# Kernel optimization log

Hardware: AMD Instinct MI355X
Metric: run time of the kernel (lower is better)

Reference implementation:

```python
import math
import jax, jax.numpy as jnp
import numpy as np

NUM_HEAD = 8
EPS = 1e-5

def _ln(v, w, b):
    m = jnp.mean(v, axis=-1, keepdims=True)
    var = jnp.var(v, axis=-1, keepdims=True)  # biased var, as torch LayerNorm
    return (v - m) * jax.lax.rsqrt(var + EPS) * w + b

def setup_inputs() -> dict:
    key = jax.random.key(0)
    ks = jax.random.split(key, 5)
    B, T, D, L, Hd = 16, 2048, 512, 768, 512
    return {
        "x": jax.random.normal(ks[0], (B, T, D), jnp.float32),
        "xf": jax.random.normal(ks[1], (B, T, L), jnp.float32),
        "norm_w": jnp.ones((D,), jnp.float32),
        "norm_b": jnp.zeros((D,), jnp.float32),
        "tnorm_w": jnp.ones((L,), jnp.float32),
        "tnorm_b": jnp.zeros((L,), jnp.float32),
        "Wq": jax.random.normal(ks[2], (Hd, D), jnp.float32) * (1.0 / math.sqrt(D)),
        "Wk": jax.random.normal(ks[3], (Hd, L), jnp.float32) * (1.0 / math.sqrt(L)),
        "Wv": jax.random.normal(ks[4], (Hd, L), jnp.float32) * (1.0 / math.sqrt(L)),
    }

def reference(x, xf, norm_w, norm_b, tnorm_w, tnorm_b, Wq, Wk, Wv):
    B, T, _ = x.shape
    Hd = Wq.shape[0]
    H = NUM_HEAD
    d = Hd // H
    q = _ln(x, norm_w, norm_b) @ Wq.T                 # B,T,Hd
    xf_n = _ln(xf, tnorm_w, tnorm_b)
    k = xf_n @ Wk.T                                   # B,T,Hd (N == T)
    v = xf_n @ Wv.T                                   # B,T,Hd
    qh = q.reshape(B, T, H, d)
    kh = k.reshape(B, T, H, d)
    vh = v.reshape(B, T, H, d)
    # per-position, per-head dot product gate (no softmax)
    w = jnp.einsum('bthd,bthd->bth', qh, kh) / math.sqrt(d)
    # dropout in eval mode = identity
    y2 = (w[..., None] * vh).reshape(B, T, Hd)
    y1 = ((1.0 - w)[..., None] * qh).reshape(B, T, Hd)
    return (y1, y2)
```

## Files before the change

kernel.cpp:

```cpp
#include <hip/hip_runtime.h>

#define NT 512
#define MT 64

typedef __attribute__((ext_vector_type(8))) short short8;
typedef __attribute__((ext_vector_type(4))) float f32x4;
typedef __attribute__((ext_vector_type(4))) unsigned short u16x4;

__device__ __forceinline__ unsigned short f2bf(float f) {
  unsigned int u = __builtin_bit_cast(unsigned int, f);
  u += 0x7fffu + ((u >> 16) & 1u);
  return (unsigned short)(u >> 16);
}
__device__ __forceinline__ float bf2f(unsigned short h) {
  return __builtin_bit_cast(float, ((unsigned int)h) << 16);
}

__global__ void cvt_weights(const float* __restrict__ wq,
                            const float* __restrict__ wk,
                            const float* __restrict__ wv,
                            unsigned short* __restrict__ o) {
  int stride = gridDim.x * blockDim.x;
  int i0 = blockIdx.x * blockDim.x + threadIdx.x;
  for (int t = i0; t < 32768; t += stride) {
    int lane = t & 63, n = (t >> 6) & 3, kk32 = (t >> 8) & 15, head = t >> 12;
    int row = head * 64 + n * 16 + (lane & 15);
    int k   = kk32 * 32 + (lane >> 4) * 8;
    const float* s = wq + (size_t)row * 512 + k;
    unsigned short* d = o + (size_t)t * 8;
    #pragma unroll
    for (int e = 0; e < 8; ++e) d[e] = f2bf(s[e]);
  }
  for (int t = i0; t < 49152; t += stride) {
    int lane = t & 63, n = (t >> 6) & 3, rem = t >> 8;
    int kk32 = rem % 24, head = rem / 24;
    int row = head * 64 + n * 16 + (lane & 15);
    int k   = kk32 * 32 + (lane >> 4) * 8;
    const float* s = wk + (size_t)row * 768 + k;
    unsigned short* d = o + 262144 + (size_t)t * 8;
    #pragma unroll
    for (int e = 0; e < 8; ++e) d[e] = f2bf(s[e]);
  }
  for (int t = i0; t < 49152; t += stride) {
    int lane = t & 63, n = (t >> 6) & 3, rem = t >> 8;
    int kk32 = rem % 24, head = rem / 24;
    int row = head * 64 + n * 16 + (lane & 15);
    int k   = kk32 * 32 + (lane >> 4) * 8;
    const float* s = wv + (size_t)row * 768 + k;
    unsigned short* d = o + 655360 + (size_t)t * 8;
    #pragma unroll
    for (int e = 0; e < 8; ++e) d[e] = f2bf(s[e]);
  }
}

__global__ __launch_bounds__(NT, 2)
void fused_xattn(const float* __restrict__ x, const float* __restrict__ xf,
                 const float* __restrict__ nw, const float* __restrict__ nb,
                 const float* __restrict__ tw, const float* __restrict__ tb,
                 const unsigned short* __restrict__ wbf,
                 float* __restrict__ out) {
  __shared__ __attribute__((aligned(16))) char ldsX[65536];
  __shared__ __attribute__((aligned(16))) char ldsF[98304];
  const int tid   = threadIdx.x;
  const int lane  = tid & 63;
  const int wid   = tid >> 6;
  const int lr    = lane & 15;
  const int lkb   = (lane >> 4) * 8;
  const int lrow4 = (lane >> 4) * 4;

  const long row0 = (long)blockIdx.x * MT;
  float* __restrict__ y1 = out;
  float* __restrict__ y2 = out + 16777216L;

  {
    const f32x4* g4 = (const f32x4*)nw;
    const f32x4* b4 = (const f32x4*)nb;
    f32x4 g0 = g4[lane], g1 = g4[lane + 64];
    f32x4 c0 = b4[lane], c1 = b4[lane + 64];
    #pragma unroll
    for (int cch = 0; cch < 2; ++cch) {
      f32x4 t0[4], t1[4];
      #pragma unroll
      for (int j = 0; j < 4; ++j) {
        const f32x4* rp = (const f32x4*)(x + (row0 + wid + 8 * (cch * 4 + j)) * 512);
        t0[j] = rp[lane]; t1[j] = rp[lane + 64];
      }
      #pragma unroll
      for (int j = 0; j < 4; ++j) {
        f32x4 a = t0[j], b = t1[j];
        float s  = a.x + a.y + a.z + a.w + b.x + b.y + b.z + b.w;
        float s2 = a.x*a.x + a.y*a.y + a.z*a.z + a.w*a.w
                 + b.x*b.x + b.y*b.y + b.z*b.z + b.w*b.w;
        #pragma unroll
        for (int m = 1; m < 64; m <<= 1) { s += __shfl_xor(s, m, 64); s2 += __shfl_xor(s2, m, 64); }
        float mean = s * (1.0f / 512.0f);
        float var  = s2 * (1.0f / 512.0f) - mean * mean;
        float rs   = rsqrtf(var + 1e-5f);
        u16x4 o0 = { f2bf((a.x - mean) * rs * g0.x + c0.x),
                     f2bf((a.y - mean) * rs * g0.y + c0.y),
                     f2bf((a.z - mean) * rs * g0.z + c0.z),
                     f2bf((a.w - mean) * rs * g0.w + c0.w) };
        u16x4 o1 = { f2bf((b.x - mean) * rs * g1.x + c1.x),
                     f2bf((b.y - mean) * rs * g1.y + c1.y),
                     f2bf((b.z - mean) * rs * g1.z + c1.z),
                     f2bf((b.w - mean) * rs * g1.w + c1.w) };
        int r = wid + 8 * (cch * 4 + j);
        int base = r * 1024, sw = (r & 7) << 4;
        *(u16x4*)(ldsX + ((base +       lane * 8) ^ sw)) = o0;
        *(u16x4*)(ldsX + ((base + 512 + lane * 8) ^ sw)) = o1;
      }
    }
  }
  __syncthreads();

  f32x4 f0[2], f1[2], f2[2];
  #pragma unroll
  for (int j = 0; j < 2; ++j) {
    const f32x4* rp = (const f32x4*)(xf + (row0 + wid + 8 * j) * 768);
    f0[j] = rp[lane]; f1[j] = rp[lane + 64]; f2[j] = rp[lane + 128];
  }

  f32x4 qa[4][4] = {};
  {
    const unsigned short* bq = wbf + wid * 32768 + lane * 8;
    short8 bc[4];
    #pragma unroll
    for (int n = 0; n < 4; ++n) bc[n] = *(const short8*)(bq + n * 512);
    for (int kk = 0; kk < 16; ++kk) {
      short8 a[4];
      #pragma unroll
      for (int m = 0; m < 4; ++m) {
        int row = m * 16 + lr;
        a[m] = *(const short8*)(ldsX + ((row * 1024 + (kk * 32 + lkb) * 2) ^ ((row & 7) << 4)));
      }
      short8 bn[4];
      if (kk < 15) {
        #pragma unroll
        for (int n = 0; n < 4; ++n) bn[n] = *(const short8*)(bq + (kk + 1) * 2048 + n * 512);
      }
      #pragma unroll
      for (int n = 0; n < 4; ++n)
        #pragma unroll
        for (int m = 0; m < 4; ++m)
          qa[m][n] = __builtin_amdgcn_mfma_f32_16x16x32_bf16(a[m], bc[n], qa[m][n], 0, 0, 0);
      if (kk < 15) {
        #pragma unroll
        for (int n = 0; n < 4; ++n) bc[n] = bn[n];
      }
    }
  }

  const f32x4* tg4 = (const f32x4*)tw;
  const f32x4* tb4 = (const f32x4*)tb;
  f32x4 tg0 = tg4[lane], tg1 = tg4[lane + 64], tg2 = tg4[lane + 128];
  f32x4 tc0 = tb4[lane], tc1 = tb4[lane + 64], tc2 = tb4[lane + 128];

#define LNF_CHUNK(c2)                                                          \
  {                                                                            \
    _Pragma("unroll")                                                          \
    for (int j = 0; j < 2; ++j) {                                              \
      f32x4 a = f0[j], b = f1[j], c = f2[j];                                   \
      float s  = a.x + a.y + a.z + a.w + b.x + b.y + b.z + b.w                 \
               + c.x + c.y + c.z + c.w;                                        \
      float s2 = a.x*a.x + a.y*a.y + a.z*a.z + a.w*a.w                         \
               + b.x*b.x + b.y*b.y + b.z*b.z + b.w*b.w                         \
               + c.x*c.x + c.y*c.y + c.z*c.z + c.w*c.w;                        \
      _Pragma("unroll")                                                        \
      for (int m = 1; m < 64; m <<= 1) {                                       \
        s += __shfl_xor(s, m, 64); s2 += __shfl_xor(s2, m, 64);                \
      }                                                                        \
      float mean = s * (1.0f / 768.0f);                                        \
      float var  = s2 * (1.0f / 768.0f) - mean * mean;                         \
      float rs   = rsqrtf(var + 1e-5f);                                        \
      u16x4 o0 = { f2bf((a.x - mean) * rs * tg0.x + tc0.x),                    \
                   f2bf((a.y - mean) * rs * tg0.y + tc0.y),                    \
                   f2bf((a.z - mean) * rs * tg0.z + tc0.z),                    \
                   f2bf((a.w - mean) * rs * tg0.w + tc0.w) };                  \
      u16x4 o1 = { f2bf((b.x - mean) * rs * tg1.x + tc1.x),                    \
                   f2bf((b.y - mean) * rs * tg1.y + tc1.y),                    \
                   f2bf((b.z - mean) * rs * tg1.z + tc1.z),                    \
                   f2bf((b.w - mean) * rs * tg1.w + tc1.w) };                  \
      u16x4 o2 = { f2bf((c.x - mean) * rs * tg2.x + tc2.x),                    \
                   f2bf((c.y - mean) * rs * tg2.y + tc2.y),                    \
                   f2bf((c.z - mean) * rs * tg2.z + tc2.z),                    \
                   f2bf((c.w - mean) * rs * tg2.w + tc2.w) };                  \
      int r = wid + 8 * ((c2) * 2 + j);                                        \
      int base = r * 1536, sw = (r & 7) << 4;                                  \
      *(u16x4*)(ldsF + ((base +        lane * 8) ^ sw)) = o0;                  \
      *(u16x4*)(ldsF + ((base + 512  + lane * 8) ^ sw)) = o1;                  \
      *(u16x4*)(ldsF + ((base + 1024 + lane * 8) ^ sw)) = o2;                  \
    }                                                                          \
  }
#define LDF_CHUNK(c2)                                                          \
  {                                                                            \
    _Pragma("unroll")                                                          \
    for (int j = 0; j < 2; ++j) {                                              \
      const f32x4* rp = (const f32x4*)(xf + (row0 + wid + 8 * ((c2) * 2 + j)) * 768); \
      f0[j] = rp[lane]; f1[j] = rp[lane + 64]; f2[j] = rp[lane + 128];         \
    }                                                                          \
  }

  {
    f32x4 n0[2], n1[2], n2[2];
    #pragma unroll
    for (int j = 0; j < 2; ++j) {
      const f32x4* rp = (const f32x4*)(xf + (row0 + wid + 8 * (2 + j)) * 768);
      n0[j] = rp[lane]; n1[j] = rp[lane + 64]; n2[j] = rp[lane + 128];
    }
    LNF_CHUNK(0)
    #pragma unroll
    for (int j = 0; j < 2; ++j) { f0[j] = n0[j]; f1[j] = n1[j]; f2[j] = n2[j]; }
  }
  __syncthreads();

  {
    unsigned long long* q8 = (unsigned long long*)ldsX;
    #pragma unroll
    for (int m = 0; m < 4; ++m)
      #pragma unroll
      for (int n = 0; n < 4; ++n) {
        unsigned long long v =
            (unsigned long long)f2bf(qa[m][n][0])
          | ((unsigned long long)f2bf(qa[m][n][1]) << 16)
          | ((unsigned long long)f2bf(qa[m][n][2]) << 32)
          | ((unsigned long long)f2bf(qa[m][n][3]) << 48);
        q8[wid * 1024 + (m * 4 + n) * 64 + lane] = v;
      }
  }

  {
    f32x4 n0[2], n1[2], n2[2];
    #pragma unroll
    for (int j = 0; j < 2; ++j) {
      const f32x4* rp = (const f32x4*)(xf + (row0 + wid + 8 * (4 + j)) * 768);
      n0[j] = rp[lane]; n1[j] = rp[lane + 64]; n2[j] = rp[lane + 128];
    }
    LNF_CHUNK(1)
    #pragma unroll
    for (int j = 0; j < 2; ++j) { f0[j] = n0[j]; f1[j] = n1[j]; f2[j] = n2[j]; }
    #pragma unroll
    for (int j = 0; j < 2; ++j) {
      const f32x4* rp = (const f32x4*)(xf + (row0 + wid + 8 * (6 + j)) * 768);
      n0[j] = rp[lane]; n1[j] = rp[lane + 64]; n2[j] = rp[lane + 128];
    }
    LNF_CHUNK(2)
    #pragma unroll
    for (int j = 0; j < 2; ++j) { f0[j] = n0[j]; f1[j] = n1[j]; f2[j] = n2[j]; }
    LNF_CHUNK(3)
  }
  __syncthreads();

  f32x4 ka[4][4] = {}, va[4][4] = {};
  {
    const unsigned short* bk = wbf + 262144 + wid * 49152 + lane * 8;
    const unsigned short* bv = wbf + 655360 + wid * 49152 + lane * 8;
    for (int kk = 0; kk < 24; ++kk) {
      short8 kf[4], vf[4];
      #pragma unroll
      for (int n = 0; n < 4; ++n) {
        kf[n] = *(const short8*)(bk + kk * 2048 + n * 512);
        vf[n] = *(const short8*)(bv + kk * 2048 + n * 512);
      }
      short8 a[4];
      #pragma unroll
      for (int m = 0; m < 4; ++m) {
        int row = m * 16 + lr;
        a[m] = *(const short8*)(ldsF + ((row * 1536 + (kk * 32 + lkb) * 2) ^ ((row & 7) << 4)));
      }
      #pragma unroll
      for (int n = 0; n < 4; ++n)
        #pragma unroll
        for (int m = 0; m < 4; ++m) {
          ka[m][n] = __builtin_amdgcn_mfma_f32_16x16x32_bf16(a[m], kf[n], ka[m][n], 0, 0, 0);
          va[m][n] = __builtin_amdgcn_mfma_f32_16x16x32_bf16(a[m], vf[n], va[m][n], 0, 0, 0);
        }
    }
  }

  unsigned long long q64[4][4];
  {
    const unsigned long long* q8 = (const unsigned long long*)ldsX;
    #pragma unroll
    for (int m = 0; m < 4; ++m)
      #pragma unroll
      for (int n = 0; n < 4; ++n)
        q64[m][n] = q8[wid * 1024 + (m * 4 + n) * 64 + lane];
  }
  float wgt[4][4];
  #pragma unroll
  for (int m = 0; m < 4; ++m) {
    #pragma unroll
    for (int r = 0; r < 4; ++r) {
      float p = 0.0f;
      #pragma unroll
      for (int n = 0; n < 4; ++n)
        p += bf2f((unsigned short)(q64[m][n] >> (16 * r))) * ka[m][n][r];
      #pragma unroll
      for (int msk = 1; msk < 16; msk <<= 1) p += __shfl_xor(p, msk, 64);
      wgt[m][r] = p * 0.125f;
    }
  }
  #pragma unroll
  for (int m = 0; m < 4; ++m) {
    #pragma unroll
    for (int r = 0; r < 4; ++r) {
      float f = 1.0f - wgt[m][r];
      long grow = row0 + m * 16 + lrow4 + r;
      #pragma unroll
      for (int n = 0; n < 4; ++n) {
        int ch = wid * 64 + n * 16 + lr;
        y1[grow * 512 + ch] = f * bf2f((unsigned short)(q64[m][n] >> (16 * r)));
      }
    }
  }
  #pragma unroll
  for (int m = 0; m < 4; ++m) {
    #pragma unroll
    for (int r = 0; r < 4; ++r) {
      float f = wgt[m][r];
      long grow = row0 + m * 16 + lrow4 + r;
      #pragma unroll
      for (int n = 0; n < 4; ++n) {
        int ch = wid * 64 + n * 16 + lr;
        y2[grow * 512 + ch] = f * va[m][n][r];
      }
    }
  }
#undef LNF_CHUNK
#undef LDF_CHUNK
}

extern "C" void kernel_launch(void* const* d_in, const int* in_sizes, int n_in,
                              void* d_out, int out_size, void* d_ws, size_t ws_size,
                              hipStream_t stream) {
  const float* x  = (const float*)d_in[0];
  const float* xf = (const float*)d_in[1];
  const float* nw = (const float*)d_in[2];
  const float* nb = (const float*)d_in[3];
  const float* tw = (const float*)d_in[4];
  const float* tb = (const float*)d_in[5];
  const float* wq = (const float*)d_in[6];
  const float* wk = (const float*)d_in[7];
  const float* wv = (const float*)d_in[8];
  unsigned short* wbf = (unsigned short*)d_ws;

  cvt_weights<<<256, 256, 0, stream>>>(wq, wk, wv, wbf);
  fused_xattn<<<512, NT, 0, stream>>>(x, xf, nw, nb, tw, tb, wbf, (float*)d_out);
}
```

Before: 125.5 us.

## Split K/V projections into column halves and keep packed Q in registers

The Q GEMM loop is fully unrolled with double-buffered weight fragments. The Q accumulator is packed to bf16 pairs in registers, so it no longer round-trips through LDS with an extra barrier. The fused K+V GEMM is split into sequential K and V passes, each over two column halves, with the per-row dot product accumulated as it goes. This reduces live accumulator registers so occupancy can rise or spills drop, at the cost of reading the LDS A-tiles four times instead of once and issuing more, smaller weight loads.

```diff
diff --git a/kernel.cpp b/kernel.cpp
--- a/kernel.cpp
+++ b/kernel.cpp
@@ -123,37 +123,76 @@
   f32x4 qa[4][4] = {};
   {
     const unsigned short* bq = wbf + wid * 32768 + lane * 8;
-    short8 bc[4];
-    #pragma unroll
-    for (int n = 0; n < 4; ++n) bc[n] = *(const short8*)(bq + n * 512);
-    for (int kk = 0; kk < 16; ++kk) {
-      short8 a[4];
-      #pragma unroll
-      for (int m = 0; m < 4; ++m) {
-        int row = m * 16 + lr;
-        a[m] = *(const short8*)(ldsX + ((row * 1024 + (kk * 32 + lkb) * 2) ^ ((row & 7) << 4)));
+    short8 b0[4], b1[4];
+    #pragma unroll
+    for (int n = 0; n < 4; ++n) {
+      b0[n] = *(const short8*)(bq + 0 * 2048 + n * 512);
+      b1[n] = *(const short8*)(bq + 1 * 2048 + n * 512);
+    }
+    #pragma unroll
+    for (int p = 0; p < 8; ++p) {
+      {
+        short8 a[4];
+        #pragma unroll
+        for (int m = 0; m < 4; ++m) {
+          int row = m * 16 + lr;
+          a[m] = *(const short8*)(ldsX + ((row * 1024 + ((2 * p) * 32 + lkb) * 2) ^ ((row & 7) << 4)));
+        }
+        short8 nb[4];
+        if (p < 7) {
+          #pragma unroll
+          for (int n = 0; n < 4; ++n) nb[n] = *(const short8*)(bq + (2 * p + 2) * 2048 + n * 512);
+        }
+        #pragma unroll
+        for (int n = 0; n < 4; ++n)
+          #pragma unroll
+          for (int m = 0; m < 4; ++m)
+            qa[m][n] = __builtin_amdgcn_mfma_f32_16x16x32_bf16(a[m], b0[n], qa[m][n], 0, 0, 0);
+        if (p < 7) {
+          #pragma unroll
+          for (int n = 0; n < 4; ++n) b0[n] = nb[n];
+        }
       }
-      short8 bn[4];
-      if (kk < 15) {
+      {
+        short8 a[4];
         #pragma unroll
-        for (int n = 0; n < 4; ++n) bn[n] = *(const short8*)(bq + (kk + 1) * 2048 + n * 512);
+        for (int m = 0; m < 4; ++m) {
+          int row = m * 16 + lr;
+          a[m] = *(const short8*)(ldsX + ((row * 1024 + ((2 * p + 1) * 32 + lkb) * 2) ^ ((row & 7) << 4)));
+        }
+        short8 nb[4];
+        if (p < 7) {
+          #pragma unroll
+          for (int n = 0; n < 4; ++n) nb[n] = *(const short8*)(bq + (2 * p + 3) * 2048 + n * 512);
+        }
+        #pragma unroll
+        for (int n = 0; n < 4; ++n)
+          #pragma unroll
+          for (int m = 0; m < 4; ++m)
+            qa[m][n] = __builtin_amdgcn_mfma_f32_16x16x32_bf16(a[m], b1[n], qa[m][n], 0, 0, 0);
+        if (p < 7) {
+          #pragma unroll
+          for (int n = 0; n < 4; ++n) b1[n] = nb[n];
+        }
       }
-      #pragma unroll
-      for (int n = 0; n < 4; ++n)
-        #pragma unroll
-        for (int m = 0; m < 4; ++m)
-          qa[m][n] = __builtin_amdgcn_mfma_f32_16x16x32_bf16(a[m], bc[n], qa[m][n], 0, 0, 0);
-      if (kk < 15) {
-        #pragma unroll
-        for (int n = 0; n < 4; ++n) bc[n] = bn[n];
-      }
-    }
-  }
-
-  const f32x4* tg4 = (const f32x4*)tw;
-  const f32x4* tb4 = (const f32x4*)tb;
-  f32x4 tg0 = tg4[lane], tg1 = tg4[lane + 64], tg2 = tg4[lane + 128];
-  f32x4 tc0 = tb4[lane], tc1 = tb4[lane + 64], tc2 = tb4[lane + 128];
+    }
+  }
+
+  unsigned q32[4][4][2];
+  #pragma unroll
+  for (int m = 0; m < 4; ++m)
+    #pragma unroll
+    for (int n = 0; n < 4; ++n) {
+      q32[m][n][0] = (unsigned)f2bf(qa[m][n][0]) | ((unsigned)f2bf(qa[m][n][1]) << 16);
+      q32[m][n][1] = (unsigned)f2bf(qa[m][n][2]) | ((unsigned)f2bf(qa[m][n][3]) << 16);
+    }
+#define QF(m, n, r) bf2f((unsigned short)(q32[m][n][(r) >> 1] >> (((r) & 1) * 16)))
+
+  {
+    const f32x4* g4 = (const f32x4*)tw;
+    const f32x4* b4 = (const f32x4*)tb;
+    f32x4 tg0 = g4[lane], tg1 = g4[lane + 64], tg2 = g4[lane + 128];
+    f32x4 tc0 = b4[lane], tc1 = b4[lane + 64], tc2 = b4[lane + 128];
 
 #define LNF_CHUNK(c2)                                                          \
   {                                                                            \
@@ -191,16 +230,7 @@
       *(u16x4*)(ldsF + ((base + 1024 + lane * 8) ^ sw)) = o2;                  \
     }                                                                          \
   }
-#define LDF_CHUNK(c2)                                                          \
-  {                                                                            \
-    _Pragma("unroll")                                                          \
-    for (int j = 0; j < 2; ++j) {                                              \
-      const f32x4* rp = (const f32x4*)(xf + (row0 + wid + 8 * ((c2) * 2 + j)) * 768); \
-      f0[j] = rp[lane]; f1[j] = rp[lane + 64]; f2[j] = rp[lane + 128];         \
-    }                                                                          \
-  }
-
-  {
+
     f32x4 n0[2], n1[2], n2[2];
     #pragma unroll
     for (int j = 0; j < 2; ++j) {
@@ -210,26 +240,6 @@
     LNF_CHUNK(0)
     #pragma unroll
     for (int j = 0; j < 2; ++j) { f0[j] = n0[j]; f1[j] = n1[j]; f2[j] = n2[j]; }
-  }
-  __syncthreads();
-
-  {
-    unsigned long long* q8 = (unsigned long long*)ldsX;
-    #pragma unroll
-    for (int m = 0; m < 4; ++m)
-      #pragma unroll
-      for (int n = 0; n < 4; ++n) {
-        unsigned long long v =
-            (unsigned long long)f2bf(qa[m][n][0])
-          | ((unsigned long long)f2bf(qa[m][n][1]) << 16)
-          | ((unsigned long long)f2bf(qa[m][n][2]) << 32)
-          | ((unsigned long long)f2bf(qa[m][n][3]) << 48);
-        q8[wid * 1024 + (m * 4 + n) * 64 + lane] = v;
-      }
-  }
-
-  {
-    f32x4 n0[2], n1[2], n2[2];
     #pragma unroll
     for (int j = 0; j < 2; ++j) {
       const f32x4* rp = (const f32x4*)(xf + (row0 + wid + 8 * (4 + j)) * 768);
@@ -247,59 +257,91 @@
     #pragma unroll
     for (int j = 0; j < 2; ++j) { f0[j] = n0[j]; f1[j] = n1[j]; f2[j] = n2[j]; }
     LNF_CHUNK(3)
+#undef LNF_CHUNK
   }
   __syncthreads();
 
-  f32x4 ka[4][4] = {}, va[4][4] = {};
-  {
-    const unsigned short* bk = wbf + 262144 + wid * 49152 + lane * 8;
-    const unsigned short* bv = wbf + 655360 + wid * 49152 + lane * 8;
-    for (int kk = 0; kk < 24; ++kk) {
-      short8 kf[4], vf[4];
-      #pragma unroll
-      for (int n = 0; n < 4; ++n) {
-        kf[n] = *(const short8*)(bk + kk * 2048 + n * 512);
-        vf[n] = *(const short8*)(bv + kk * 2048 + n * 512);
-      }
-      short8 a[4];
-      #pragma unroll
-      for (int m = 0; m < 4; ++m) {
-        int row = m * 16 + lr;
-        a[m] = *(const short8*)(ldsF + ((row * 1536 + (kk * 32 + lkb) * 2) ^ ((row & 7) << 4)));
-      }
-      #pragma unroll
-      for (int n = 0; n < 4; ++n)
-        #pragma unroll
-        for (int m = 0; m < 4; ++m) {
-          ka[m][n] = __builtin_amdgcn_mfma_f32_16x16x32_bf16(a[m], kf[n], ka[m][n], 0, 0, 0);
-          va[m][n] = __builtin_amdgcn_mfma_f32_16x16x32_bf16(a[m], vf[n], va[m][n], 0, 0, 0);
-        }
-    }
-  }
-
-  unsigned long long q64[4][4];
-  {
-    const unsigned long long* q8 = (const unsigned long long*)ldsX;
-    #pragma unroll
-    for (int m = 0; m < 4; ++m)
-      #pragma unroll
-      for (int n = 0; n < 4; ++n)
-        q64[m][n] = q8[wid * 1024 + (m * 4 + n) * 64 + lane];
-  }
+  float pp[4][4];
+  #pragma unroll
+  for (int m = 0; m < 4; ++m)
+    #pragma unroll
+    for (int r = 0; r < 4; ++r) pp[m][r] = 0.0f;
+
+#define KHALF(H)                                                               \
+  {                                                                            \
+    const unsigned short* bk = wbf + 262144 + wid * 49152 + (H) * 1024 + lane * 8; \
+    f32x4 ka[4][2] = {};                                                       \
+    short8 b0[2], b1[2];                                                       \
+    _Pragma("unroll")                                                          \
+    for (int n = 0; n < 2; ++n) {                                              \
+      b0[n] = *(const short8*)(bk + 0 * 2048 + n * 512);                       \
+      b1[n] = *(const short8*)(bk + 1 * 2048 + n * 512);                       \
+    }                                                                          \
+    _Pragma("unroll")                                                          \
+    for (int p = 0; p < 12; ++p) {                                             \
+      {                                                                        \
+        short8 a[4];                                                           \
+        _Pragma("unroll")                                                      \
+        for (int m = 0; m < 4; ++m) {                                          \
+          int row = m * 16 + lr;                                               \
+          a[m] = *(const short8*)(ldsF + ((row * 1536 + ((2 * p) * 32 + lkb) * 2) ^ ((row & 7) << 4))); \
+        }                                                                      \
+        short8 nb[2];                                                          \
+        if (p < 11) {                                                          \
+          _Pragma("unroll")                                                    \
+          for (int n = 0; n < 2; ++n) nb[n] = *(const short8*)(bk + (2 * p + 2) * 2048 + n * 512); \
+        }                                                                      \
+        _Pragma("unroll")                                                      \
+        for (int n = 0; n < 2; ++n)                                            \
+          _Pragma("unroll")                                                    \
+          for (int m = 0; m < 4; ++m)                                          \
+            ka[m][n] = __builtin_amdgcn_mfma_f32_16x16x32_bf16(a[m], b0[n], ka[m][n], 0, 0, 0); \
+        if (p < 11) { b0[0] = nb[0]; b0[1] = nb[1]; }                          \
+      }                                                                        \
+      {                                                                        \
+        short8 a[4];                                                           \
+        _Pragma("unroll")                                                      \
+        for (int m = 0; m < 4; ++m) {                                          \
+          int row = m * 16 + lr;                                               \
+          a[m] = *(const short8*)(ldsF + ((row * 1536 + ((2 * p + 1) * 32 + lkb) * 2) ^ ((row & 7) << 4))); \
+        }                                                                      \
+        short8 nb[2];                                                          \
+        if (p < 11) {                                                          \
+          _Pragma("unroll")                                                    \
+          for (int n = 0; n < 2; ++n) nb[n] = *(const short8*)(bk + (2 * p + 3) * 2048 + n * 512); \
+        }                                                                      \
+        _Pragma("unroll")                                                      \
+        for (int n = 0; n < 2; ++n)                                            \
+          _Pragma("unroll")                                                    \
+          for (int m = 0; m < 4; ++m)                                          \
+            ka[m][n] = __builtin_amdgcn_mfma_f32_16x16x32_bf16(a[m], b1[n], ka[m][n], 0, 0, 0); \
+        if (p < 11) { b1[0] = nb[0]; b1[1] = nb[1]; }                          \
+      }                                                                        \
+    }                                                                          \
+    _Pragma("unroll")                                                          \
+    for (int m = 0; m < 4; ++m)                                                \
+      _Pragma("unroll")                                                        \
+      for (int r = 0; r < 4; ++r)                                              \
+        pp[m][r] += QF(m, (H) * 2, r) * ka[m][0][r]                            \
+                  + QF(m, (H) * 2 + 1, r) * ka[m][1][r];                       \
+  }
+
+  KHALF(0)
+  KHALF(1)
+#undef KHALF
+
   float wgt[4][4];
   #pragma unroll
   for (int m = 0; m < 4; ++m) {
     #pragma unroll
     for (int r = 0; r < 4; ++r) {
-      float p = 0.0f;
-      #pragma unroll
-      for (int n = 0; n < 4; ++n)
-        p += bf2f((unsigned short)(q64[m][n] >> (16 * r))) * ka[m][n][r];
+      float p = pp[m][r];
       #pragma unroll
       for (int msk = 1; msk < 16; msk <<= 1) p += __shfl_xor(p, msk, 64);
       wgt[m][r] = p * 0.125f;
     }
   }
+
   #pragma unroll
   for (int m = 0; m < 4; ++m) {
     #pragma unroll
@@ -309,25 +351,81 @@
       #pragma unroll
       for (int n = 0; n < 4; ++n) {
         int ch = wid * 64 + n * 16 + lr;
-        y1[grow * 512 + ch] = f * bf2f((unsigned short)(q64[m][n] >> (16 * r)));
+        y1[grow * 512 + ch] = f * QF(m, n, r);
       }
     }
   }
-  #pragma unroll
-  for (int m = 0; m < 4; ++m) {
-    #pragma unroll
-    for (int r = 0; r < 4; ++r) {
-      float f = wgt[m][r];
-      long grow = row0 + m * 16 + lrow4 + r;
-      #pragma unroll
-      for (int n = 0; n < 4; ++n) {
-        int ch = wid * 64 + n * 16 + lr;
-        y2[grow * 512 + ch] = f * va[m][n][r];
-      }
-    }
-  }
-#undef LNF_CHUNK
-#undef LDF_CHUNK
+
+#define VHALF(H)                                                               \
+  {                                                                            \
+    const unsigned short* bv = wbf + 655360 + wid * 49152 + (H) * 1024 + lane * 8; \
+    f32x4 va[4][2] = {};                                                       \
+    short8 b0[2], b1[2];                                                       \
+    _Pragma("unroll")                                                          \
+    for (int n = 0; n < 2; ++n) {                                              \
+      b0[n] = *(const short8*)(bv + 0 * 2048 + n * 512);                       \
+      b1[n] = *(const short8*)(bv + 1 * 2048 + n * 512);                       \
+    }                                                                          \
+    _Pragma("unroll")                                                          \
+    for (int p = 0; p < 12; ++p) {                                             \
+      {                                                                        \
+        short8 a[4];                                                           \
+        _Pragma("unroll")                                                      \
+        for (int m = 0; m < 4; ++m) {                                          \
+          int row = m * 16 + lr;                                               \
+          a[m] = *(const short8*)(ldsF + ((row * 1536 + ((2 * p) * 32 + lkb) * 2) ^ ((row & 7) << 4))); \
+        }                                                                      \
+        short8 nb[2];                                                          \
+        if (p < 11) {                                                          \
+          _Pragma("unroll")                                                    \
+          for (int n = 0; n < 2; ++n) nb[n] = *(const short8*)(bv + (2 * p + 2) * 2048 + n * 512); \
+        }                                                                      \
+        _Pragma("unroll")                                                      \
+        for (int n = 0; n < 2; ++n)                                            \
+          _Pragma("unroll")                                                    \
+          for (int m = 0; m < 4; ++m)                                          \
+            va[m][n] = __builtin_amdgcn_mfma_f32_16x16x32_bf16(a[m], b0[n], va[m][n], 0, 0, 0); \
+        if (p < 11) { b0[0] = nb[0]; b0[1] = nb[1]; }                          \
+      }                                                                        \
+      {                                                                        \
+        short8 a[4];                                                           \
+        _Pragma("unroll")                                                      \
+        for (int m = 0; m < 4; ++m) {                                          \
+          int row = m * 16 + lr;                                               \
+          a[m] = *(const short8*)(ldsF + ((row * 1536 + ((2 * p + 1) * 32 + lkb) * 2) ^ ((row & 7) << 4))); \
+        }                                                                      \
+        short8 nb[2];                                                          \
+        if (p < 11) {                                                          \
+          _Pragma("unroll")                                                    \
+          for (int n = 0; n < 2; ++n) nb[n] = *(const short8*)(bv + (2 * p + 3) * 2048 + n * 512); \
+        }                                                                      \
+        _Pragma("unroll")                                                      \
+        for (int n = 0; n < 2; ++n)                                            \
+          _Pragma("unroll")                                                    \
+          for (int m = 0; m < 4; ++m)                                          \
+            va[m][n] = __builtin_amdgcn_mfma_f32_16x16x32_bf16(a[m], b1[n], va[m][n], 0, 0, 0); \
+        if (p < 11) { b1[0] = nb[0]; b1[1] = nb[1]; }                          \
+      }                                                                        \
+    }                                                                          \
+    _Pragma("unroll")                                                          \
+    for (int m = 0; m < 4; ++m) {                                              \
+      _Pragma("unroll")                                                        \
+      for (int r = 0; r < 4; ++r) {                                            \
+        float f = wgt[m][r];                                                   \
+        long grow = row0 + m * 16 + lrow4 + r;                                 \
+        _Pragma("unroll")                                                      \
+        for (int n = 0; n < 2; ++n) {                                          \
+          int ch = wid * 64 + ((H) * 2 + n) * 16 + lr;                         \
+          y2[grow * 512 + ch] = f * va[m][n][r];                               \
+        }                                                                      \
+      }                                                                        \
+    }                                                                          \
+  }
+
+  VHALF(0)
+  VHALF(1)
+#undef VHALF
+#undef QF
 }
 
 extern "C" void kernel_launch(void* const* d_in, const int* in_sizes, int n_in,
```

Result: slower. 202.9 us (+61.7%).
